# Kernel tuning notes

Measured on AMD Instinct MI355X. Metric: run time of the kernel, lower is better.

The kernel has to match this reference:

```python
import jax, jax.numpy as jnp
import numpy as np


def setup_inputs() -> dict:
    key = jax.random.key(0)
    k_x, k_g, k_fc, k_pj = jax.random.split(key, 4)
    B, T, C, H, E = 4, 2048, 1024, 2048, 8
    n_layer = 12
    x = jax.random.normal(k_x, (B, T, C), dtype=jnp.float32)
    w_gate = 0.02 * jax.random.normal(k_g, (C, E), dtype=jnp.float32)
    w_fc = 0.02 * jax.random.normal(k_fc, (C, H, E), dtype=jnp.float32)
    w_proj = (0.02 * (2 * n_layer) ** -0.5) * jax.random.normal(k_pj, (H, C, E), dtype=jnp.float32)
    return {"x": x, "w_gate": w_gate, "w_fc": w_fc, "w_proj": w_proj, "top_k": 2}


def reference(x, w_gate, w_fc, w_proj, top_k):
    # x: (B,T,C); w_gate: (C,E); w_fc: (C,H,E); w_proj: (H,C,E)
    E = w_gate.shape[-1]
    gate = jnp.einsum('btc,ce->bte', x, w_gate)                  # gating logits
    top_vals, top_idx = jax.lax.top_k(gate, top_k)               # (B,T,K) — raw logits used as combine weights (as in source)
    # Per-expert combine weight: sum_k top_val_k * onehot(idx_k) — zero for unselected experts.
    # This is mathematically identical to gathering the K expert weight slices per token
    # (the source's gather+einsum) but avoids the (B,T,C,H,K) weight blowup.
    onehot = jax.nn.one_hot(top_idx, E, dtype=x.dtype)           # (B,T,K,E)
    w_e = jnp.einsum('btk,btke->bte', top_vals, onehot)          # (B,T,E)
    h = jax.nn.silu(jnp.einsum('btc,che->bthe', x, w_fc))        # (B,T,H,E)
    o = jnp.einsum('bthe,bte,hce->btc', h, w_e, w_proj)          # weighted expert combine
    return o
```

## Files before the change

### kernel.cpp

```cpp
#include <hip/hip_runtime.h>
#include <hip/hip_bf16.h>


#define NTOK 8192
#define CD   1024
#define HD   2048
#define NE   8
#define NSLOT 16384
#define MT256 10
#define BK   64
#define NT1  (CD / BK)
#define NT2  (HD / BK)
#define PACK_BLOCKS 2048

typedef short  short4_t  __attribute__((ext_vector_type(4)));
typedef short  short8_t  __attribute__((ext_vector_type(8)));
typedef __bf16 bf16x8_t  __attribute__((ext_vector_type(8)));
typedef float  f32x4_t   __attribute__((ext_vector_type(4)));

struct FragArg {
  short8_t v;
  __device__ operator short8_t() const { return v; }
  __device__ operator bf16x8_t() const { return __builtin_bit_cast(bf16x8_t, v); }
};

static __device__ __forceinline__ float b2f(unsigned short u) {
  union { float f; unsigned int i; } w; w.i = ((unsigned int)u) << 16; return w.f;
}
static __device__ __forceinline__ unsigned short f2b(float f) {
  unsigned int u = __float_as_uint(f);
  u += 0x7fffu + ((u >> 16) & 1u);
  return (unsigned short)(u >> 16);
}
static __device__ __forceinline__ void gl2lds16(const void* g, void* l) {
  __builtin_amdgcn_global_load_lds((__attribute__((address_space(1))) void*)g,
                                   (__attribute__((address_space(3))) void*)l,
                                   16, 0, 0);
}

static __device__ __forceinline__ void pack_tile(
    const float* __restrict__ in, unsigned short* __restrict__ out,
    int D0, int D1, int b0, int b1, unsigned short* smem, int t)
{
  int d1i = t & 31, d0q = t >> 5;
  #pragma unroll
  for (int r = 0; r < 4; ++r) {
    int d0i = d0q * 4 + r;
    const float* src = in + ((size_t)(b0 + d0i) * D1 + (b1 + d1i)) * NE;
    float4 v0 = *(const float4*)src;
    float4 v1 = *(const float4*)(src + 4);
    unsigned short* dst0 = &smem[d1i * 40 + d0i];
    dst0[0 * 32 * 40] = f2b(v0.x);
    dst0[1 * 32 * 40] = f2b(v0.y);
    dst0[2 * 32 * 40] = f2b(v0.z);
    dst0[3 * 32 * 40] = f2b(v0.w);
    dst0[4 * 32 * 40] = f2b(v1.x);
    dst0[5 * 32 * 40] = f2b(v1.y);
    dst0[6 * 32 * 40] = f2b(v1.z);
    dst0[7 * 32 * 40] = f2b(v1.w);
  }
  __syncthreads();
  int dchunk = t & 3, d1w = (t >> 2) & 31, ehalf = t >> 7;
  #pragma unroll
  for (int p = 0; p < 4; ++p) {
    int e = ehalf + 2 * p;
    short8_t v = *(const short8_t*)&smem[e * 32 * 40 + d1w * 40 + dchunk * 8];
    *(short8_t*)(out + ((size_t)e * D1 + (b1 + d1w)) * D0 + b0 + dchunk * 8) = v;
  }
}

#define GATE_BLOCKS (NTOK / 4)
__global__ __launch_bounds__(256) void prep_kernel(
    const float* __restrict__ x, const float* __restrict__ wg,
    const float* __restrict__ wfc, const float* __restrict__ wpj,
    unsigned short* __restrict__ xb, unsigned short* __restrict__ wfcp,
    unsigned short* __restrict__ wpjp,
    int* __restrict__ tok_e, float* __restrict__ tok_v,
    int* __restrict__ g_counts)
{
  __shared__ __align__(16) unsigned short lds[NE * 32 * 40];
  __shared__ int hist[NE];
  int t = threadIdx.x;

  if (blockIdx.x < GATE_BLOCKS) {
    if (t < NE) hist[t] = 0;
    __syncthreads();
    int wv = t >> 6, lane = t & 63;
    int tk = blockIdx.x * 4 + wv;
    const float* xr = x + (size_t)tk * CD;
    unsigned short* xbr = xb + (size_t)tk * CD;
    float acc[NE] = {0, 0, 0, 0, 0, 0, 0, 0};
    #pragma unroll
    for (int jj = 0; jj < 4; ++jj) {
      int c0 = (lane + 64 * jj) * 4;
      float4 xv = *(const float4*)(xr + c0);
      short4_t ob;
      ob[0] = (short)f2b(xv.x); ob[1] = (short)f2b(xv.y);
      ob[2] = (short)f2b(xv.z); ob[3] = (short)f2b(xv.w);
      *(short4_t*)(xbr + c0) = ob;
      #pragma unroll
      for (int j = 0; j < 4; ++j) {
        float xf = (j == 0) ? xv.x : (j == 1) ? xv.y : (j == 2) ? xv.z : xv.w;
        const float* wr = wg + (size_t)(c0 + j) * NE;
        float4 w0 = *(const float4*)wr;
        float4 w1 = *(const float4*)(wr + 4);
        acc[0] += xf * w0.x; acc[1] += xf * w0.y;
        acc[2] += xf * w0.z; acc[3] += xf * w0.w;
        acc[4] += xf * w1.x; acc[5] += xf * w1.y;
        acc[6] += xf * w1.z; acc[7] += xf * w1.w;
      }
    }
    #pragma unroll
    for (int off = 32; off >= 1; off >>= 1)
      #pragma unroll
      for (int e = 0; e < NE; ++e) acc[e] += __shfl_down(acc[e], off, 64);
    if (lane == 0) {
      float v1 = -3.0e38f, v2 = -3.0e38f; int i1 = 0, i2 = 1;
      #pragma unroll
      for (int e = 0; e < NE; ++e) {
        float g = acc[e];
        if (g > v1) { v2 = v1; i2 = i1; v1 = g; i1 = e; }
        else if (g > v2) { v2 = g; i2 = e; }
      }
      tok_e[tk * 2] = i1; tok_e[tk * 2 + 1] = i2;
      tok_v[tk * 2] = v1; tok_v[tk * 2 + 1] = v2;
      atomicAdd(&hist[i1], 1); atomicAdd(&hist[i2], 1);
    }
    __syncthreads();
    if (t < NE && hist[t] > 0) atomicAdd(&g_counts[t], hist[t]);
  } else if (blockIdx.x < GATE_BLOCKS + PACK_BLOCKS) {
    int pid = blockIdx.x - GATE_BLOCKS;
    int bx = pid & 63, by = pid >> 6;
    pack_tile(wfc, wfcp, CD, HD, by * 32, bx * 32, lds, t);
  } else {
    int pid = blockIdx.x - GATE_BLOCKS - PACK_BLOCKS;
    int bx = pid & 63, by = pid >> 6;
    pack_tile(wpj, wpjp, HD, CD, bx * 32, by * 32, lds, t);
  }
}

__global__ __launch_bounds__(256) void scatter_kernel(
    const int* __restrict__ tok_e, const float* __restrict__ tok_v,
    const int* __restrict__ g_counts, int* __restrict__ g_cursor,
    int* __restrict__ g_base,
    int* __restrict__ bucket_tok, float* __restrict__ bucket_v,
    int* __restrict__ slot_of)
{
  int gid = blockIdx.x * 256 + threadIdx.x;
  int lane = threadIdx.x & 63;
  int base[NE];
  { int o = 0;
    #pragma unroll
    for (int e = 0; e < NE; ++e) { base[e] = o; o += g_counts[e]; } }
  int e = tok_e[gid];
  unsigned long long lanebit = 1ull << lane;
  int pos = 0;
  #pragma unroll
  for (int ee = 0; ee < NE; ++ee) {
    unsigned long long m = __ballot(e == ee);
    if (e == ee) {
      int leader = __ffsll((long long)m) - 1;
      int cnt = __popcll(m);
      int start = 0;
      if (lane == leader) start = atomicAdd(&g_cursor[ee], cnt);
      start = __shfl(start, leader, 64);
      pos = start + __popcll(m & (lanebit - 1));
    }
  }
  int sl = base[e] + pos;
  bucket_tok[sl] = gid >> 1;
  bucket_v[sl]   = tok_v[gid];
  slot_of[gid]   = sl;
  if (gid < NE) g_base[gid] = base[gid];
}

__global__ __launch_bounds__(512, 2) void gemm1_kernel(
    const unsigned short* __restrict__ xb, const unsigned short* __restrict__ wfcp,
    const int* __restrict__ g_counts, const int* __restrict__ g_base,
    const int* __restrict__ bucket_tok, const float* __restrict__ bucket_v,
    unsigned short* __restrict__ hbuf)
{
  __shared__ __align__(16) unsigned short lsA[2][2][256][32];
  __shared__ __align__(16) unsigned short lsB[2][2][256][32];
  __shared__ int   s_tok[256];
  __shared__ float s_v[256];

  int id = blockIdx.x;
  int e = id & 7;
  int r = id >> 3;
  int nt = r & 7;
  int mt = r >> 3;

  int cnt = g_counts[e];
  int m0 = mt * 256;
  if (m0 >= cnt) return;
  int base = g_base[e];
  int n0 = nt * 256;

  int t = threadIdx.x;
  if (t < 256) {
    int ok = (m0 + t) < cnt;
    s_tok[t] = ok ? bucket_tok[base + m0 + t] : 0;
    s_v[t]   = ok ? bucket_v[base + m0 + t] : 0.0f;
  }
  __syncthreads();

  int lane = t & 63, w = t >> 6;
  int w32 = w * 32;
  int rl0 = w32 + (lane >> 2);
  int rl1 = rl0 + 16;
  int cb  = ((lane & 3) ^ (rl0 & 3)) * 8;
  const unsigned short* aS0 = xb + (size_t)s_tok[rl0] * CD + cb;
  const unsigned short* aS1 = xb + (size_t)s_tok[rl1] * CD + cb;
  const unsigned short* bS0 = wfcp + ((size_t)e * HD + n0 + rl0) * CD + cb;
  const unsigned short* bS1 = wfcp + ((size_t)e * HD + n0 + rl1) * CD + cb;

  #define STGA1(tt, kh) do {                                             \
    int _ko = (tt) * BK + (kh) * 32;                                     \
    gl2lds16(aS0 + _ko, &lsA[(tt) & 1][kh][w32][0]);                     \
    gl2lds16(aS1 + _ko, &lsA[(tt) & 1][kh][w32 + 16][0]);                \
  } while (0)
  #define STGB1(tt, kh) do {                                             \
    int _ko = (tt) * BK + (kh) * 32;                                     \
    gl2lds16(bS0 + _ko, &lsB[(tt) & 1][kh][w32][0]);                     \
    gl2lds16(bS1 + _ko, &lsB[(tt) & 1][kh][w32 + 16][0]);                \
  } while (0)

  int wr = w >> 2, wc = w & 3;
  int ml = lane & 15, kq = lane >> 4;
  int sw8 = (kq ^ (ml & 3)) * 8;

  f32x4_t acc[8][4];
  #pragma unroll
  for (int i = 0; i < 8; ++i)
    #pragma unroll
    for (int j = 0; j < 4; ++j) acc[i][j] = (f32x4_t){0.f, 0.f, 0.f, 0.f};

  STGA1(0, 0); STGB1(0, 0); STGA1(0, 1); STGB1(0, 1);

  #pragma unroll 1
  for (int tt = 0; tt < NT1; ++tt) {
    int buf = tt & 1;
    short8_t af[4], bfr[4];
    asm volatile("s_waitcnt vmcnt(4)" ::: "memory");
    __builtin_amdgcn_s_barrier();
    asm volatile("" ::: "memory");
    #pragma unroll
    for (int i = 0; i < 4; ++i)
      af[i]  = *(const short8_t*)&lsA[buf][0][wr * 128 + i * 16 + ml][sw8];
    #pragma unroll
    for (int j = 0; j < 4; ++j)
      bfr[j] = *(const short8_t*)&lsB[buf][0][wc * 64 + j * 16 + ml][sw8];
    if (tt + 1 < NT1) STGA1(tt + 1, 0);
    __builtin_amdgcn_s_setprio(1);
    #pragma unroll
    for (int i = 0; i < 4; ++i)
      #pragma unroll
      for (int j = 0; j < 4; ++j)
        acc[i][j] = __builtin_amdgcn_mfma_f32_16x16x32_bf16(
            FragArg{af[i]}, FragArg{bfr[j]}, acc[i][j], 0, 0, 0);
    __builtin_amdgcn_s_setprio(0);
    #pragma unroll
    for (int i = 0; i < 4; ++i)
      af[i]  = *(const short8_t*)&lsA[buf][0][wr * 128 + 64 + i * 16 + ml][sw8];
    if (tt + 1 < NT1) STGB1(tt + 1, 0);
    __builtin_amdgcn_s_setprio(1);
    #pragma unroll
    for (int i = 0; i < 4; ++i)
      #pragma unroll
      for (int j = 0; j < 4; ++j)
        acc[4 + i][j] = __builtin_amdgcn_mfma_f32_16x16x32_bf16(
            FragArg{af[i]}, FragArg{bfr[j]}, acc[4 + i][j], 0, 0, 0);
    __builtin_amdgcn_s_setprio(0);
    if (tt + 1 < NT1) asm volatile("s_waitcnt vmcnt(4)" ::: "memory");
    else              asm volatile("s_waitcnt vmcnt(0)" ::: "memory");
    __builtin_amdgcn_s_barrier();
    asm volatile("" ::: "memory");
    #pragma unroll
    for (int i = 0; i < 4; ++i)
      af[i]  = *(const short8_t*)&lsA[buf][1][wr * 128 + i * 16 + ml][sw8];
    #pragma unroll
    for (int j = 0; j < 4; ++j)
      bfr[j] = *(const short8_t*)&lsB[buf][1][wc * 64 + j * 16 + ml][sw8];
    if (tt + 1 < NT1) STGA1(tt + 1, 1);
    __builtin_amdgcn_s_setprio(1);
    #pragma unroll
    for (int i = 0; i < 4; ++i)
      #pragma unroll
      for (int j = 0; j < 4; ++j)
        acc[i][j] = __builtin_amdgcn_mfma_f32_16x16x32_bf16(
            FragArg{af[i]}, FragArg{bfr[j]}, acc[i][j], 0, 0, 0);
    __builtin_amdgcn_s_setprio(0);
    #pragma unroll
    for (int i = 0; i < 4; ++i)
      af[i]  = *(const short8_t*)&lsA[buf][1][wr * 128 + 64 + i * 16 + ml][sw8];
    if (tt + 1 < NT1) STGB1(tt + 1, 1);
    __builtin_amdgcn_s_setprio(1);
    #pragma unroll
    for (int i = 0; i < 4; ++i)
      #pragma unroll
      for (int j = 0; j < 4; ++j)
        acc[4 + i][j] = __builtin_amdgcn_mfma_f32_16x16x32_bf16(
            FragArg{af[i]}, FragArg{bfr[j]}, acc[4 + i][j], 0, 0, 0);
    __builtin_amdgcn_s_setprio(0);
  }
  #undef STGA1
  #undef STGB1

  #pragma unroll
  for (int i = 0; i < 8; ++i) {
    int rb = wr * 128 + i * 16 + kq * 4;
    #pragma unroll
    for (int r2 = 0; r2 < 4; ++r2) {
      int row = rb + r2;
      if (m0 + row < cnt) {
        float v = s_v[row];
        size_t ro = (size_t)(base + m0 + row) * HD + n0;
        #pragma unroll
        for (int j = 0; j < 4; ++j) {
          float z = acc[i][j][r2];
          float val = v * (z / (1.0f + __expf(-z)));
          hbuf[ro + wc * 64 + j * 16 + ml] = f2b(val);
        }
      }
    }
  }
}

__global__ __launch_bounds__(512, 2) void gemm2_kernel(
    const unsigned short* __restrict__ hbuf, const unsigned short* __restrict__ wpjp,
    const int* __restrict__ g_counts, const int* __restrict__ g_base,
    unsigned short* __restrict__ oslot)
{
  __shared__ __align__(16) unsigned short lsA[2][2][256][32];
  __shared__ __align__(16) unsigned short lsB[2][2][256][32];

  int id = blockIdx.x;
  int e = id & 7;
  int r = id >> 3;
  int nt = r & 3;
  int mt = r >> 2;

  int cnt = g_counts[e];
  int m0 = mt * 256;
  if (m0 >= cnt) return;
  int base = g_base[e];
  int n0 = nt * 256;

  int t = threadIdx.x;
  int lane = t & 63, w = t >> 6;
  int w32 = w * 32;
  int rl0 = w32 + (lane >> 2);
  int rl1 = rl0 + 16;
  int cb  = ((lane & 3) ^ (rl0 & 3)) * 8;
  const unsigned short* aS0 = hbuf + ((size_t)(base + m0 + rl0)) * HD + cb;
  const unsigned short* aS1 = hbuf + ((size_t)(base + m0 + rl1)) * HD + cb;
  const unsigned short* bS0 = wpjp + ((size_t)e * CD + n0 + rl0) * HD + cb;
  const unsigned short* bS1 = wpjp + ((size_t)e * CD + n0 + rl1) * HD + cb;

  #define STGA2(tt, kh) do {                                             \
    int _ko = (tt) * BK + (kh) * 32;                                     \
    gl2lds16(aS0 + _ko, &lsA[(tt) & 1][kh][w32][0]);                     \
    gl2lds16(aS1 + _ko, &lsA[(tt) & 1][kh][w32 + 16][0]);                \
  } while (0)
  #define STGB2(tt, kh) do {                                             \
    int _ko = (tt) * BK + (kh) * 32;                                     \
    gl2lds16(bS0 + _ko, &lsB[(tt) & 1][kh][w32][0]);                     \
    gl2lds16(bS1 + _ko, &lsB[(tt) & 1][kh][w32 + 16][0]);                \
  } while (0)

  int wr = w >> 2, wc = w & 3;
  int ml = lane & 15, kq = lane >> 4;
  int sw8 = (kq ^ (ml & 3)) * 8;

  f32x4_t acc[8][4];
  #pragma unroll
  for (int i = 0; i < 8; ++i)
    #pragma unroll
    for (int j = 0; j < 4; ++j) acc[i][j] = (f32x4_t){0.f, 0.f, 0.f, 0.f};

  asm volatile("s_waitcnt vmcnt(0)" ::: "memory");
  STGA2(0, 0); STGB2(0, 0); STGA2(0, 1); STGB2(0, 1);

  #pragma unroll 1
  for (int tt = 0; tt < NT2; ++tt) {
    int buf = tt & 1;
    short8_t af[4], bfr[4];
    asm volatile("s_waitcnt vmcnt(4)" ::: "memory");
    __builtin_amdgcn_s_barrier();
    asm volatile("" ::: "memory");
    #pragma unroll
    for (int i = 0; i < 4; ++i)
      af[i]  = *(const short8_t*)&lsA[buf][0][wr * 128 + i * 16 + ml][sw8];
    #pragma unroll
    for (int j = 0; j < 4; ++j)
      bfr[j] = *(const short8_t*)&lsB[buf][0][wc * 64 + j * 16 + ml][sw8];
    if (tt + 1 < NT2) STGA2(tt + 1, 0);
    __builtin_amdgcn_s_setprio(1);
    #pragma unroll
    for (int i = 0; i < 4; ++i)
      #pragma unroll
      for (int j = 0; j < 4; ++j)
        acc[i][j] = __builtin_amdgcn_mfma_f32_16x16x32_bf16(
            FragArg{af[i]}, FragArg{bfr[j]}, acc[i][j], 0, 0, 0);
    __builtin_amdgcn_s_setprio(0);
    #pragma unroll
    for (int i = 0; i < 4; ++i)
      af[i]  = *(const short8_t*)&lsA[buf][0][wr * 128 + 64 + i * 16 + ml][sw8];
    if (tt + 1 < NT2) STGB2(tt + 1, 0);
    __builtin_amdgcn_s_setprio(1);
    #pragma unroll
    for (int i = 0; i < 4; ++i)
      #pragma unroll
      for (int j = 0; j < 4; ++j)
        acc[4 + i][j] = __builtin_amdgcn_mfma_f32_16x16x32_bf16(
            FragArg{af[i]}, FragArg{bfr[j]}, acc[4 + i][j], 0, 0, 0);
    __builtin_amdgcn_s_setprio(0);
    if (tt + 1 < NT2) asm volatile("s_waitcnt vmcnt(4)" ::: "memory");
    else              asm volatile("s_waitcnt vmcnt(0)" ::: "memory");
    __builtin_amdgcn_s_barrier();
    asm volatile("" ::: "memory");
    #pragma unroll
    for (int i = 0; i < 4; ++i)
      af[i]  = *(const short8_t*)&lsA[buf][1][wr * 128 + i * 16 + ml][sw8];
    #pragma unroll
    for (int j = 0; j < 4; ++j)
      bfr[j] = *(const short8_t*)&lsB[buf][1][wc * 64 + j * 16 + ml][sw8];
    if (tt + 1 < NT2) STGA2(tt + 1, 1);
    __builtin_amdgcn_s_setprio(1);
    #pragma unroll
    for (int i = 0; i < 4; ++i)
      #pragma unroll
      for (int j = 0; j < 4; ++j)
        acc[i][j] = __builtin_amdgcn_mfma_f32_16x16x32_bf16(
            FragArg{af[i]}, FragArg{bfr[j]}, acc[i][j], 0, 0, 0);
    __builtin_amdgcn_s_setprio(0);
    #pragma unroll
    for (int i = 0; i < 4; ++i)
      af[i]  = *(const short8_t*)&lsA[buf][1][wr * 128 + 64 + i * 16 + ml][sw8];
    if (tt + 1 < NT2) STGB2(tt + 1, 1);
    __builtin_amdgcn_s_setprio(1);
    #pragma unroll
    for (int i = 0; i < 4; ++i)
      #pragma unroll
      for (int j = 0; j < 4; ++j)
        acc[4 + i][j] = __builtin_amdgcn_mfma_f32_16x16x32_bf16(
            FragArg{af[i]}, FragArg{bfr[j]}, acc[4 + i][j], 0, 0, 0);
    __builtin_amdgcn_s_setprio(0);
  }
  #undef STGA2
  #undef STGB2

  #pragma unroll
  for (int i = 0; i < 8; ++i) {
    int rb = wr * 128 + i * 16 + kq * 4;
    #pragma unroll
    for (int r2 = 0; r2 < 4; ++r2) {
      int row = rb + r2;
      if (m0 + row < cnt) {
        size_t ro = (size_t)(base + m0 + row) * CD + n0;
        #pragma unroll
        for (int j = 0; j < 4; ++j)
          oslot[ro + wc * 64 + j * 16 + ml] = f2b(acc[i][j][r2]);
      }
    }
  }
}

__global__ __launch_bounds__(256) void combine_kernel(
    const unsigned short* __restrict__ oslot, const int* __restrict__ slot_of,
    float* __restrict__ out)
{
  int gid = blockIdx.x * 256 + threadIdx.x;
  int tk = gid >> 7;
  int ch = (gid & 127) * 8;
  int s0 = slot_of[tk * 2], s1 = slot_of[tk * 2 + 1];
  short8_t a = *(const short8_t*)(oslot + (size_t)s0 * CD + ch);
  short8_t b = *(const short8_t*)(oslot + (size_t)s1 * CD + ch);
  float* op = out + (size_t)tk * CD + ch;
  float4 o0, o1;
  o0.x = b2f((unsigned short)a[0]) + b2f((unsigned short)b[0]);
  o0.y = b2f((unsigned short)a[1]) + b2f((unsigned short)b[1]);
  o0.z = b2f((unsigned short)a[2]) + b2f((unsigned short)b[2]);
  o0.w = b2f((unsigned short)a[3]) + b2f((unsigned short)b[3]);
  o1.x = b2f((unsigned short)a[4]) + b2f((unsigned short)b[4]);
  o1.y = b2f((unsigned short)a[5]) + b2f((unsigned short)b[5]);
  o1.z = b2f((unsigned short)a[6]) + b2f((unsigned short)b[6]);
  o1.w = b2f((unsigned short)a[7]) + b2f((unsigned short)b[7]);
  *(float4*)op = o0;
  *(float4*)(op + 4) = o1;
}

extern "C" void kernel_launch(void* const* d_in, const int* in_sizes, int n_in,
                              void* d_out, int out_size, void* d_ws, size_t ws_size,
                              hipStream_t stream)
{
  const float* x   = (const float*)d_in[0];
  const float* wg  = (const float*)d_in[1];
  const float* wfc = (const float*)d_in[2];
  const float* wpj = (const float*)d_in[3];
  float* out = (float*)d_out;

  char* w = (char*)d_ws;
  unsigned short* wfcp  = (unsigned short*)w; w += (size_t)NE * HD * CD * 2;
  unsigned short* wpjp  = (unsigned short*)w; w += (size_t)NE * CD * HD * 2;
  unsigned short* xb    = (unsigned short*)w; w += (size_t)NTOK * CD * 2;
  unsigned short* hbuf  = (unsigned short*)w; w += (size_t)NSLOT * HD * 2;
  unsigned short* oslot = (unsigned short*)w; w += (size_t)NSLOT * CD * 2;
  int*   tok_e      = (int*)w;   w += NSLOT * 4;
  float* tok_v      = (float*)w; w += NSLOT * 4;
  int*   slot_of    = (int*)w;   w += NSLOT * 4;
  int*   bucket_tok = (int*)w;   w += NSLOT * 4;
  float* bucket_v   = (float*)w; w += NSLOT * 4;
  int*   g_counts   = (int*)w;   w += NE * 4;
  int*   g_cursor   = (int*)w;   w += NE * 4;
  int*   g_base     = (int*)w;   w += 256;

  hipMemsetAsync(g_counts, 0, 2 * NE * sizeof(int), stream);
  prep_kernel<<<GATE_BLOCKS + 2 * PACK_BLOCKS, 256, 0, stream>>>(
      x, wg, wfc, wpj, xb, wfcp, wpjp, tok_e, tok_v, g_counts);
  scatter_kernel<<<NSLOT / 256, 256, 0, stream>>>(
      tok_e, tok_v, g_counts, g_cursor, g_base, bucket_tok, bucket_v, slot_of);
  gemm1_kernel<<<(HD / 256) * MT256 * NE, 512, 0, stream>>>(
      xb, wfcp, g_counts, g_base, bucket_tok, bucket_v, hbuf);
  gemm2_kernel<<<(CD / 256) * MT256 * NE, 512, 0, stream>>>(
      hbuf, wpjp, g_counts, g_base, oslot);
  combine_kernel<<<(NTOK * CD / 8) / 256, 256, 0, stream>>>(oslot, slot_of, out);
}
```

Measured before the change: 468.2 us.

## Schedule GEMM tiles from a compacted tile list and change LDS swizzle

The scatter kernel now builds a compact list of (expert, m-tile) pairs, with full tiles first and partial tiles last. Both GEMM kernels map block IDs through this list, so live tiles are packed at the front of the grid and dead blocks exit at the tail. The order of n-tiles relative to m-tiles also changes, which affects L2 reuse of activations versus weights. Separately, the LDS XOR swizzle pattern is changed on both the write and read sides, meant to reduce bank conflicts.

```diff
diff --git a/kernel.cpp b/kernel.cpp
--- a/kernel.cpp
+++ b/kernel.cpp
@@ -12,6 +12,7 @@
 #define NT1  (CD / BK)
 #define NT2  (HD / BK)
 #define PACK_BLOCKS 2048
+#define MAXTILES (NE * MT256)
 
 typedef short  short4_t  __attribute__((ext_vector_type(4)));
 typedef short  short8_t  __attribute__((ext_vector_type(8)));
@@ -144,7 +145,7 @@
     const int* __restrict__ g_counts, int* __restrict__ g_cursor,
     int* __restrict__ g_base,
     int* __restrict__ bucket_tok, float* __restrict__ bucket_v,
-    int* __restrict__ slot_of)
+    int* __restrict__ slot_of, int* __restrict__ tlist)
 {
   int gid = blockIdx.x * 256 + threadIdx.x;
   int lane = threadIdx.x & 63;
@@ -172,12 +173,45 @@
   bucket_v[sl]   = tok_v[gid];
   slot_of[gid]   = sl;
   if (gid < NE) g_base[gid] = base[gid];
+
+  if (blockIdx.x == 0 && threadIdx.x < MAXTILES) {
+    int gi = threadIdx.x;
+    int nfull[NE], npart[NE];
+    int tot_full = 0;
+    #pragma unroll
+    for (int ee = 0; ee < NE; ++ee) {
+      int c = g_counts[ee];
+      int f = c >> 8;
+      int p = ((c & 255) != 0) ? 1 : 0;
+      if (f + p > MT256) { f = MT256; p = 0; }
+      nfull[ee] = f; npart[ee] = p;
+      tot_full += f;
+    }
+    int val = -1;
+    if (gi < tot_full) {
+      int acc = 0;
+      #pragma unroll
+      for (int ee = 0; ee < NE; ++ee) {
+        if (gi >= acc && gi < acc + nfull[ee]) val = (ee << 16) | (gi - acc);
+        acc += nfull[ee];
+      }
+    } else {
+      int idx = gi - tot_full, acc = 0;
+      #pragma unroll
+      for (int ee = 0; ee < NE; ++ee) {
+        if (npart[ee] && idx == acc) val = (ee << 16) | nfull[ee];
+        acc += npart[ee];
+      }
+    }
+    tlist[gi] = val;
+  }
 }
 
 __global__ __launch_bounds__(512, 2) void gemm1_kernel(
     const unsigned short* __restrict__ xb, const unsigned short* __restrict__ wfcp,
     const int* __restrict__ g_counts, const int* __restrict__ g_base,
     const int* __restrict__ bucket_tok, const float* __restrict__ bucket_v,
+    const int* __restrict__ tlist,
     unsigned short* __restrict__ hbuf)
 {
   __shared__ __align__(16) unsigned short lsA[2][2][256][32];
@@ -186,10 +220,11 @@
   __shared__ float s_v[256];
 
   int id = blockIdx.x;
-  int e = id & 7;
-  int r = id >> 3;
-  int nt = r & 7;
-  int mt = r >> 3;
+  int nt = id & 7;
+  int ti = id >> 3;
+  int tv = tlist[ti];
+  if (tv < 0) return;
+  int e = tv >> 16, mt = tv & 0xffff;
 
   int cnt = g_counts[e];
   int m0 = mt * 256;
@@ -209,7 +244,7 @@
   int w32 = w * 32;
   int rl0 = w32 + (lane >> 2);
   int rl1 = rl0 + 16;
-  int cb  = ((lane & 3) ^ (rl0 & 3)) * 8;
+  int cb  = ((lane & 3) ^ ((lane >> 3) & 3)) * 8;
   const unsigned short* aS0 = xb + (size_t)s_tok[rl0] * CD + cb;
   const unsigned short* aS1 = xb + (size_t)s_tok[rl1] * CD + cb;
   const unsigned short* bS0 = wfcp + ((size_t)e * HD + n0 + rl0) * CD + cb;
@@ -228,7 +263,7 @@
 
   int wr = w >> 2, wc = w & 3;
   int ml = lane & 15, kq = lane >> 4;
-  int sw8 = (kq ^ (ml & 3)) * 8;
+  int sw8 = (kq ^ ((ml >> 1) & 3)) * 8;
 
   f32x4_t acc[8][4];
   #pragma unroll
@@ -262,7 +297,7 @@
     __builtin_amdgcn_s_setprio(0);
     #pragma unroll
     for (int i = 0; i < 4; ++i)
-      af[i]  = *(const short8_t*)&lsA[buf][0][wr * 128 + 64 + i * 16 + ml][sw8];
+      af[i] = *(const short8_t*)&lsA[buf][0][wr * 128 + 64 + i * 16 + ml][sw8];
     if (tt + 1 < NT1) STGB1(tt + 1, 0);
     __builtin_amdgcn_s_setprio(1);
     #pragma unroll
@@ -293,7 +328,7 @@
     __builtin_amdgcn_s_setprio(0);
     #pragma unroll
     for (int i = 0; i < 4; ++i)
-      af[i]  = *(const short8_t*)&lsA[buf][1][wr * 128 + 64 + i * 16 + ml][sw8];
+      af[i] = *(const short8_t*)&lsA[buf][1][wr * 128 + 64 + i * 16 + ml][sw8];
     if (tt + 1 < NT1) STGB1(tt + 1, 1);
     __builtin_amdgcn_s_setprio(1);
     #pragma unroll
@@ -330,16 +365,18 @@
 __global__ __launch_bounds__(512, 2) void gemm2_kernel(
     const unsigned short* __restrict__ hbuf, const unsigned short* __restrict__ wpjp,
     const int* __restrict__ g_counts, const int* __restrict__ g_base,
+    const int* __restrict__ tlist,
     unsigned short* __restrict__ oslot)
 {
   __shared__ __align__(16) unsigned short lsA[2][2][256][32];
   __shared__ __align__(16) unsigned short lsB[2][2][256][32];
 
   int id = blockIdx.x;
-  int e = id & 7;
-  int r = id >> 3;
-  int nt = r & 3;
-  int mt = r >> 2;
+  int nt = id & 3;
+  int ti = id >> 2;
+  int tv = tlist[ti];
+  if (tv < 0) return;
+  int e = tv >> 16, mt = tv & 0xffff;
 
   int cnt = g_counts[e];
   int m0 = mt * 256;
@@ -352,7 +389,7 @@
   int w32 = w * 32;
   int rl0 = w32 + (lane >> 2);
   int rl1 = rl0 + 16;
-  int cb  = ((lane & 3) ^ (rl0 & 3)) * 8;
+  int cb  = ((lane & 3) ^ ((lane >> 3) & 3)) * 8;
   const unsigned short* aS0 = hbuf + ((size_t)(base + m0 + rl0)) * HD + cb;
   const unsigned short* aS1 = hbuf + ((size_t)(base + m0 + rl1)) * HD + cb;
   const unsigned short* bS0 = wpjp + ((size_t)e * CD + n0 + rl0) * HD + cb;
@@ -371,7 +408,7 @@
 
   int wr = w >> 2, wc = w & 3;
   int ml = lane & 15, kq = lane >> 4;
-  int sw8 = (kq ^ (ml & 3)) * 8;
+  int sw8 = (kq ^ ((ml >> 1) & 3)) * 8;
 
   f32x4_t acc[8][4];
   #pragma unroll
@@ -406,7 +443,7 @@
     __builtin_amdgcn_s_setprio(0);
     #pragma unroll
     for (int i = 0; i < 4; ++i)
-      af[i]  = *(const short8_t*)&lsA[buf][0][wr * 128 + 64 + i * 16 + ml][sw8];
+      af[i] = *(const short8_t*)&lsA[buf][0][wr * 128 + 64 + i * 16 + ml][sw8];
     if (tt + 1 < NT2) STGB2(tt + 1, 0);
     __builtin_amdgcn_s_setprio(1);
     #pragma unroll
@@ -437,7 +474,7 @@
     __builtin_amdgcn_s_setprio(0);
     #pragma unroll
     for (int i = 0; i < 4; ++i)
-      af[i]  = *(const short8_t*)&lsA[buf][1][wr * 128 + 64 + i * 16 + ml][sw8];
+      af[i] = *(const short8_t*)&lsA[buf][1][wr * 128 + 64 + i * 16 + ml][sw8];
     if (tt + 1 < NT2) STGB2(tt + 1, 1);
     __builtin_amdgcn_s_setprio(1);
     #pragma unroll
@@ -515,15 +552,17 @@
   int*   g_counts   = (int*)w;   w += NE * 4;
   int*   g_cursor   = (int*)w;   w += NE * 4;
   int*   g_base     = (int*)w;   w += 256;
+  int*   tlist      = (int*)w;   w += 512;
 
   hipMemsetAsync(g_counts, 0, 2 * NE * sizeof(int), stream);
   prep_kernel<<<GATE_BLOCKS + 2 * PACK_BLOCKS, 256, 0, stream>>>(
       x, wg, wfc, wpj, xb, wfcp, wpjp, tok_e, tok_v, g_counts);
   scatter_kernel<<<NSLOT / 256, 256, 0, stream>>>(
-      tok_e, tok_v, g_counts, g_cursor, g_base, bucket_tok, bucket_v, slot_of);
-  gemm1_kernel<<<(HD / 256) * MT256 * NE, 512, 0, stream>>>(
-      xb, wfcp, g_counts, g_base, bucket_tok, bucket_v, hbuf);
-  gemm2_kernel<<<(CD / 256) * MT256 * NE, 512, 0, stream>>>(
-      hbuf, wpjp, g_counts, g_base, oslot);
+      tok_e, tok_v, g_counts, g_cursor, g_base, bucket_tok, bucket_v,
+      slot_of, tlist);
+  gemm1_kernel<<<MAXTILES * (HD / 256), 512, 0, stream>>>(
+      xb, wfcp, g_counts, g_base, bucket_tok, bucket_v, tlist, hbuf);
+  gemm2_kernel<<<MAXTILES * (CD / 256), 512, 0, stream>>>(
+      hbuf, wpjp, g_counts, g_base, tlist, oslot);
   combine_kernel<<<(NTOK * CD / 8) / 256, 256, 0, stream>>>(oslot, slot_of, out);
 }
```

New measurement: 472.2 us. About the same (+0.8%).
